# Optimization experiments

Hardware: AMD Instinct MI355X
Metric: run time of the kernel (lower is better)

The kernel has to match this reference:

```python
import jax, jax.numpy as jnp
import numpy as np

D_MODEL = 2048
N_HEADS = 16
N_KV_HEADS = 4
HEAD_DIM = D_MODEL // N_HEADS  # 128
SWA_WINDOW = 1024
SINK_TOKENS = 4
ROPE_BASE = 10000.0
EPS = 1e-6


def setup_inputs() -> dict:
    key = jax.random.key(0)
    ks = jax.random.split(key, 6)
    s = 0.02
    B, T = 1, 4096
    return {
        "x": jax.random.normal(ks[0], (B, T, D_MODEL), dtype=jnp.float32),
        "wq": jax.random.normal(ks[1], (N_HEADS * HEAD_DIM, D_MODEL), dtype=jnp.float32) * s,
        "wk": jax.random.normal(ks[2], (N_KV_HEADS * HEAD_DIM, D_MODEL), dtype=jnp.float32) * s,
        "wv": jax.random.normal(ks[3], (N_KV_HEADS * HEAD_DIM, D_MODEL), dtype=jnp.float32) * s,
        "wo": jax.random.normal(ks[4], (D_MODEL, D_MODEL), dtype=jnp.float32) * s,
        "qk_weight": jnp.ones((HEAD_DIM,), dtype=jnp.float32),
        "layer_idx": 1,
    }


def _rope_cos_sin(T, dtype):
    half = HEAD_DIM // 2
    inv_freq = 1.0 / (ROPE_BASE ** (jnp.arange(half, dtype=dtype) / half))
    freqs = jnp.arange(T, dtype=dtype)[:, None] * inv_freq[None, :]  # [T, half]
    return jnp.cos(freqs), jnp.sin(freqs)


def _rot(x, cos, sin):
    # x: [B,H,T,D]; cos/sin: [T,D/2]
    half = HEAD_DIM // 2
    x1, x2 = x[..., :half], x[..., half:]
    return jnp.concatenate([x1 * cos - x2 * sin, x1 * sin + x2 * cos], axis=-1)


def _qknorm(x, w):
    rms = jnp.sqrt(jnp.mean(x * x, axis=-1, keepdims=True) + EPS)
    return x / rms * w


def reference(x, wq, wk, wv, wo, qk_weight, layer_idx):
    B, T, C = x.shape
    rep = N_HEADS // N_KV_HEADS
    q = (x @ wq.T).reshape(B, T, N_HEADS, HEAD_DIM).transpose(0, 2, 1, 3)      # [B,H,T,D]
    k = (x @ wk.T).reshape(B, T, N_KV_HEADS, HEAD_DIM).transpose(0, 2, 1, 3)   # [B,Hkv,T,D]
    v = (x @ wv.T).reshape(B, T, N_KV_HEADS, HEAD_DIM).transpose(0, 2, 1, 3)
    k = jnp.repeat(k, rep, axis=1)  # GQA expand, matches repeat_interleave
    v = jnp.repeat(v, rep, axis=1)

    cos, sin = _rope_cos_sin(T, x.dtype)
    q = _rot(q, cos, sin)
    k = _rot(k, cos, sin)

    q = _qknorm(q, qk_weight)
    k = _qknorm(k, qk_weight)

    # sliding-window + sink mask (non-global layer). NOTE: faithful to the
    # original, which passes ~allowed as the boolean keep-mask to SDPA.
    i = jnp.arange(T)[:, None]
    j = jnp.arange(T)[None, :]
    allowed = (j <= i) & (((i - j) < SWA_WINDOW) | (j < SINK_TOKENS))
    keep = ~allowed  # True = attend (SDPA bool-mask semantics)

    scale = HEAD_DIM ** -0.5
    scores = jnp.einsum('bhqd,bhkd->bhqk', q, k) * scale
    scores = jnp.where(keep[None, None], scores, -jnp.inf)
    attn = jax.nn.softmax(scores, axis=-1)
    y = jnp.einsum('bhqk,bhkd->bhqd', attn, v)
    y = y.transpose(0, 2, 1, 3).reshape(B, T, C)
    return y @ wo.T
```

## Files before the change

kernel.cpp:

```cpp
#include <hip/hip_runtime.h>

typedef unsigned short u16;
typedef __bf16 bf16x8_t __attribute__((ext_vector_type(8)));
typedef float f32x4 __attribute__((ext_vector_type(4)));
typedef u16 u16x8 __attribute__((ext_vector_type(8)));
typedef u16 u16x4 __attribute__((ext_vector_type(4)));

__device__ __forceinline__ u16 f2bf(float f) {
  union { float f; unsigned u; } v; v.f = f;
  unsigned r = v.u + 0x7FFFu + ((v.u >> 16) & 1u);
  return (u16)(r >> 16);
}
__device__ __forceinline__ float bf2f(u16 b) {
  union { unsigned u; float f; } v; v.u = ((unsigned)b) << 16;
  return v.f;
}
__device__ __forceinline__ f32x4 mfma_bf16(u16x8 a, u16x8 b, f32x4 c) {
  return __builtin_amdgcn_mfma_f32_16x16x32_bf16(
      __builtin_bit_cast(bf16x8_t, a), __builtin_bit_cast(bf16x8_t, b), c, 0, 0, 0);
}

__global__ void k_cvt(const float* __restrict__ src, u16* __restrict__ dst, int n4) {
  int i = blockIdx.x * blockDim.x + threadIdx.x;
  if (i >= n4) return;
  float4 v = reinterpret_cast<const float4*>(src)[i];
  u16x4 o = { f2bf(v.x), f2bf(v.y), f2bf(v.z), f2bf(v.w) };
  reinterpret_cast<u16x4*>(dst)[i] = o;
}

template<bool BF16OUT>
__global__ __launch_bounds__(256, 2)
void k_gemm_bt(const u16* __restrict__ A, const u16* __restrict__ B,
               void* __restrict__ Cv, int M, int N, int K) {
  __shared__ u16 lA[128 * 64];
  __shared__ u16 lB[128 * 64];
  const int bm = blockIdx.y, bn = blockIdx.x;
  const int tid = threadIdx.x;
  const int wid = tid >> 6, lane = tid & 63;
  const int lo = lane & 15, hi = lane >> 4;
  const int wrow = (wid >> 1) * 64, wcol = (wid & 1) * 64;
  f32x4 acc[4][4] = {};
  const size_t abase = (size_t)(bm * 128) * K;
  const size_t bbase = (size_t)(bn * 128) * K;
  for (int kt = 0; kt < K; kt += 64) {
#pragma unroll
    for (int rr = 0; rr < 4; ++rr) {
      int e = (rr * 256 + tid) * 8;
      int row = e >> 6, col = e & 63;
      u16x8 va = *reinterpret_cast<const u16x8*>(A + abase + (size_t)row * K + kt + col);
      u16x8 vb = *reinterpret_cast<const u16x8*>(B + bbase + (size_t)row * K + kt + col);
      int sw = ((row * 64 + col) * 2) ^ ((row & 7) << 4);
      *reinterpret_cast<u16x8*>(reinterpret_cast<char*>(lA) + sw) = va;
      *reinterpret_cast<u16x8*>(reinterpret_cast<char*>(lB) + sw) = vb;
    }
    __syncthreads();
#pragma unroll
    for (int ks = 0; ks < 64; ks += 32) {
      u16x8 af[4], bfr[4];
#pragma unroll
      for (int mi = 0; mi < 4; ++mi) {
        int row = wrow + mi * 16 + lo, col = ks + hi * 8;
        int sw = ((row * 64 + col) * 2) ^ ((row & 7) << 4);
        af[mi] = *reinterpret_cast<const u16x8*>(reinterpret_cast<char*>(lA) + sw);
      }
#pragma unroll
      for (int ni = 0; ni < 4; ++ni) {
        int row = wcol + ni * 16 + lo, col = ks + hi * 8;
        int sw = ((row * 64 + col) * 2) ^ ((row & 7) << 4);
        bfr[ni] = *reinterpret_cast<const u16x8*>(reinterpret_cast<char*>(lB) + sw);
      }
#pragma unroll
      for (int mi = 0; mi < 4; ++mi)
#pragma unroll
        for (int ni = 0; ni < 4; ++ni)
          acc[mi][ni] = mfma_bf16(af[mi], bfr[ni], acc[mi][ni]);
    }
    __syncthreads();
  }
#pragma unroll
  for (int mi = 0; mi < 4; ++mi)
#pragma unroll
    for (int ni = 0; ni < 4; ++ni)
#pragma unroll
      for (int r = 0; r < 4; ++r) {
        int row = bm * 128 + wrow + mi * 16 + hi * 4 + r;
        int col = bn * 128 + wcol + ni * 16 + lo;
        if (BF16OUT)
          ((u16*)Cv)[(size_t)row * N + col] = f2bf(acc[mi][ni][r]);
        else
          ((float*)Cv)[(size_t)row * N + col] = acc[mi][ni][r];
      }
}

__global__ void k_rope_norm(const u16* __restrict__ QKV, const float* __restrict__ qkw,
                            u16* __restrict__ qb, u16* __restrict__ kb) {
  int gw = blockIdx.x * 4 + (threadIdx.x >> 6);
  int lane = threadIdx.x & 63;
  int t = gw / 20, hh = gw - t * 20;
  const u16* src = QKV + (size_t)t * 3072 + (hh < 16 ? hh * 128 : 2048 + (hh - 16) * 128);
  float x1 = bf2f(src[lane]), x2 = bf2f(src[lane + 64]);
  float invf = exp2f(-(float)lane * (13.287712379549449f / 64.0f));
  float fr = (float)t * invf;
  float sn, cs;
  sincosf(fr, &sn, &cs);
  float o1 = x1 * cs - x2 * sn, o2 = x1 * sn + x2 * cs;
  float ss = o1 * o1 + o2 * o2;
#pragma unroll
  for (int off = 32; off > 0; off >>= 1) ss += __shfl_xor(ss, off);
  float inv = rsqrtf(ss * (1.0f / 128.0f) + 1e-6f);
  o1 *= inv * qkw[lane];
  o2 *= inv * qkw[lane + 64];
  u16* dst = (hh < 16) ? (qb + ((size_t)hh * 4096 + t) * 128)
                       : (kb + ((size_t)(hh - 16) * 4096 + t) * 128);
  dst[lane] = f2bf(o1);
  dst[lane + 64] = f2bf(o2);
}

__global__ void k_transpose_v(const u16* __restrict__ QKV, u16* __restrict__ vtb) {
  __shared__ float lt[64][65];
  int b = blockIdx.x;
  int dt = b & 1, tt = (b >> 1) & 63, kv = b >> 7;
  int tid = threadIdx.x;
#pragma unroll
  for (int rr = 0; rr < 16; ++rr) {
    int row = rr * 4 + (tid >> 6);
    int col = tid & 63;
    lt[row][col] = bf2f(QKV[(size_t)(tt * 64 + row) * 3072 + 2560 + kv * 128 + dt * 64 + col]);
  }
  __syncthreads();
#pragma unroll
  for (int pp = 0; pp < 2; ++pp) {
    int idx = pp * 256 + tid;
    int dr = idx >> 3, tc = (idx & 7) * 8;
    u16x8 o;
#pragma unroll
    for (int i = 0; i < 8; ++i) o[i] = f2bf(lt[tc + i][dr]);
    *reinterpret_cast<u16x8*>(vtb + (size_t)(kv * 128 + dt * 64 + dr) * 4096 + tt * 64 + tc) = o;
  }
}

#define ATT_SL2E 0.12754276432973518f
#define ATT_SH   11.541560327111707f
#define KPAD 136
#define VPAD 40

__global__ __launch_bounds__(256)
void k_attn_mfma(const u16* __restrict__ qb, const u16* __restrict__ kb,
                 const u16* __restrict__ vtb, u16* __restrict__ yb) {
  __shared__ u16 sK[2][32][KPAD];
  __shared__ u16 sV[2][128][VPAD];
  const int h = blockIdx.y, qt = blockIdx.x;
  const int kvh = h >> 2;
  const int tid = threadIdx.x;
  const int wid = tid >> 6, lane = tid & 63;
  const int lo = lane & 15, hi = lane >> 4;
  const int q0 = qt * 128;
  const int qwA = q0 + wid * 16;
  const int qwB = qwA + 64;
  const int qrowA = qwA + lo, qrowB = qwB + lo;
  const u16* qpA = qb + ((size_t)h * 4096 + qrowA) * 128;
  const u16* qpB = qb + ((size_t)h * 4096 + qrowB) * 128;
  u16x8 qfA[4], qfB[4];
#pragma unroll
  for (int dc = 0; dc < 4; ++dc) {
    qfA[dc] = *reinterpret_cast<const u16x8*>(qpA + dc * 32 + hi * 8);
    qfB[dc] = *reinterpret_cast<const u16x8*>(qpB + dc * 32 + hi * 8);
  }
  f32x4 accOA[8] = {}, accOB[8] = {};
  float lsA = 0.0f, lsB = 0.0f;
  const u16* kbase = kb + (size_t)kvh * 4096 * 128;
  const u16* vb = vtb + (size_t)kvh * 128 * 4096;

  int past_tiles = 0;
  const int pe = q0 + 127 - 1024;
  if (pe >= 4) past_tiles = (pe >> 5) + 1;
  const int fstart = (q0 + 1) >> 5;
  const int ntiles = past_tiles + (128 - fstart);

  u16x8 kr[2], vr[2];
#define STAGE_LOAD(KT)                                                          \
  {                                                                             \
    const int kt_ = (KT);                                                       \
    _Pragma("unroll")                                                           \
    for (int p = 0; p < 2; ++p) {                                               \
      const int c = tid + p * 256;                                              \
      kr[p] = *reinterpret_cast<const u16x8*>(                                  \
          kbase + (size_t)(kt_ * 32 + (c >> 4)) * 128 + (c & 15) * 8);          \
      vr[p] = *reinterpret_cast<const u16x8*>(                                  \
          vb + (size_t)(c >> 2) * 4096 + kt_ * 32 + (c & 3) * 8);               \
    }                                                                           \
  }
#define STAGE_WRITE(BUF)                                                        \
  {                                                                             \
    const int b_ = (BUF);                                                       \
    _Pragma("unroll")                                                           \
    for (int p = 0; p < 2; ++p) {                                               \
      const int c = tid + p * 256;                                              \
      *reinterpret_cast<u16x8*>(&sK[b_][c >> 4][(c & 15) * 8]) = kr[p];         \
      const int d_ = c >> 2, a_ = c & 3;                                        \
      const int posA = ((a_ & 1) << 4) | ((a_ >> 1) << 2);                      \
      u16x4 v0_ = { vr[p][0], vr[p][1], vr[p][2], vr[p][3] };                   \
      u16x4 v1_ = { vr[p][4], vr[p][5], vr[p][6], vr[p][7] };                   \
      *reinterpret_cast<u16x4*>(&sV[b_][d_][posA]) = v0_;                       \
      *reinterpret_cast<u16x4*>(&sV[b_][d_][posA + 8]) = v1_;                   \
    }                                                                           \
  }

  STAGE_LOAD(0 < past_tiles ? 0 : fstart);
  STAGE_WRITE(0);
  __syncthreads();

  for (int i = 0; i < ntiles; ++i) {
    const int cur = i & 1;
    const int kt = (i < past_tiles) ? i : fstart + (i - past_tiles);
    const bool more = (i + 1) < ntiles;
    if (more) {
      const int i1 = i + 1;
      STAGE_LOAD((i1 < past_tiles) ? i1 : fstart + (i1 - past_tiles));
    }
    f32x4 aSA[2] = {}, aSB[2] = {};
#pragma unroll
    for (int sub = 0; sub < 2; ++sub)
#pragma unroll
      for (int dc = 0; dc < 4; ++dc) {
        u16x8 kf = *reinterpret_cast<const u16x8*>(&sK[cur][sub * 16 + lo][dc * 32 + hi * 8]);
        aSA[sub] = mfma_bf16(kf, qfA[dc], aSA[sub]);
        aSB[sub] = mfma_bf16(kf, qfB[dc], aSB[sub]);
      }
    u16x8 pfA, pfB;
#pragma unroll
    for (int sub = 0; sub < 2; ++sub)
#pragma unroll
      for (int r = 0; r < 4; ++r) {
        const int j = kt * 32 + sub * 16 + hi * 4 + r;
        float argA = aSA[sub][r] * ATT_SL2E - ATT_SH;
        float argB = aSB[sub][r] * ATT_SL2E - ATT_SH;
        const bool okA = (j > qrowA) || (((qrowA - j) >= 1024) && (j >= 4));
        const bool okB = (j > qrowB) || (((qrowB - j) >= 1024) && (j >= 4));
        argA = okA ? argA : -100000.0f;
        argB = okB ? argB : -100000.0f;
        float pA = exp2f(argA), pB = exp2f(argB);
        lsA += pA; lsB += pB;
        pfA[sub * 4 + r] = f2bf(pA);
        pfB[sub * 4 + r] = f2bf(pB);
      }
#pragma unroll
    for (int nt = 0; nt < 8; ++nt) {
      u16x8 vf = *reinterpret_cast<const u16x8*>(&sV[cur][nt * 16 + lo][hi * 8]);
      accOA[nt] = mfma_bf16(pfA, vf, accOA[nt]);
      accOB[nt] = mfma_bf16(pfB, vf, accOB[nt]);
    }
    if (more) STAGE_WRITE(cur ^ 1);
    __syncthreads();
  }
#undef STAGE_LOAD
#undef STAGE_WRITE

  lsA += __shfl_xor(lsA, 16); lsA += __shfl_xor(lsA, 32);
  lsB += __shfl_xor(lsB, 16); lsB += __shfl_xor(lsB, 32);
  float lrA[4], lrB[4];
#pragma unroll
  for (int r = 0; r < 4; ++r) {
    lrA[r] = 1.0f / __shfl(lsA, hi * 4 + r);
    lrB[r] = 1.0f / __shfl(lsB, hi * 4 + r);
  }
#pragma unroll
  for (int nt = 0; nt < 8; ++nt)
#pragma unroll
    for (int r = 0; r < 4; ++r) {
      const int tA = qwA + hi * 4 + r;
      const int tB = qwB + hi * 4 + r;
      yb[(size_t)tA * 2048 + h * 128 + nt * 16 + lo] = f2bf(accOA[nt][r] * lrA[r]);
      yb[(size_t)tB * 2048 + h * 128 + nt * 16 + lo] = f2bf(accOB[nt][r] * lrB[r]);
    }
}

extern "C" void kernel_launch(void* const* d_in, const int* in_sizes, int n_in,
                              void* d_out, int out_size, void* d_ws, size_t ws_size,
                              hipStream_t stream) {
  const float* x   = (const float*)d_in[0];
  const float* wq  = (const float*)d_in[1];
  const float* wk  = (const float*)d_in[2];
  const float* wv  = (const float*)d_in[3];
  const float* wo  = (const float*)d_in[4];
  const float* qkw = (const float*)d_in[5];
  (void)in_sizes; (void)n_in; (void)out_size; (void)ws_size;

  char* ws = (char*)d_ws;
  u16* xb    = (u16*)(ws);
  u16* wqkvb = (u16*)(ws + (16ull << 20));
  u16* wob   = (u16*)(ws + (28ull << 20));
  u16* qkvb  = (u16*)(ws + (36ull << 20));
  u16* qb    = (u16*)(ws + (60ull << 20));
  u16* kb    = (u16*)(ws + (76ull << 20));
  u16* vtb   = (u16*)(ws + (80ull << 20));
  u16* yb    = (u16*)(ws + (84ull << 20));

  k_cvt<<<8192, 256, 0, stream>>>(x, xb, 8388608 / 4);
  k_cvt<<<4096, 256, 0, stream>>>(wq, wqkvb, 4194304 / 4);
  k_cvt<<<1024, 256, 0, stream>>>(wk, wqkvb + 4194304, 1048576 / 4);
  k_cvt<<<1024, 256, 0, stream>>>(wv, wqkvb + 5242880, 1048576 / 4);
  k_cvt<<<4096, 256, 0, stream>>>(wo, wob, 4194304 / 4);

  k_gemm_bt<true><<<dim3(24, 32), 256, 0, stream>>>(xb, wqkvb, qkvb, 4096, 3072, 2048);
  k_rope_norm<<<20480, 256, 0, stream>>>(qkvb, qkw, qb, kb);
  k_transpose_v<<<512, 256, 0, stream>>>(qkvb, vtb);
  k_attn_mfma<<<dim3(32, 16), 256, 0, stream>>>(qb, kb, vtb, yb);
  k_gemm_bt<false><<<dim3(16, 32), 256, 0, stream>>>(yb, wob, (float*)d_out, 4096, 2048, 2048);
}
```

Measured before the change: 369.8 us.

## Split attention KV range across two blocks and merge partial sums

Adds a split-KV mode where each query tile's key range is divided between two blocks along grid z, each writing unnormalized fp32 partial outputs and row sums to workspace. A new merge kernel adds the two partials, normalizes, and writes bf16 output. This doubles attention grid parallelism and balances uneven tile counts, at the cost of extra fp32 global traffic and an additional launch. The split path is only taken when the workspace is large enough.

```diff
diff --git a/kernel.cpp b/kernel.cpp
--- a/kernel.cpp
+++ b/kernel.cpp
@@ -144,9 +144,11 @@
 #define KPAD 136
 #define VPAD 40
 
+template<bool SPLIT>
 __global__ __launch_bounds__(256)
 void k_attn_mfma(const u16* __restrict__ qb, const u16* __restrict__ kb,
-                 const u16* __restrict__ vtb, u16* __restrict__ yb) {
+                 const u16* __restrict__ vtb, u16* __restrict__ yb,
+                 float* __restrict__ P, float* __restrict__ L) {
   __shared__ u16 sK[2][32][KPAD];
   __shared__ u16 sV[2][128][VPAD];
   const int h = blockIdx.y, qt = blockIdx.x;
@@ -176,6 +178,12 @@
   if (pe >= 4) past_tiles = (pe >> 5) + 1;
   const int fstart = (q0 + 1) >> 5;
   const int ntiles = past_tiles + (128 - fstart);
+  int i0 = 0, i1 = ntiles;
+  if (SPLIT) {
+    const int half = blockIdx.z;
+    i0 = (half * ntiles) >> 1;
+    i1 = ((half + 1) * ntiles) >> 1;
+  }
 
   u16x8 kr[2], vr[2];
 #define STAGE_LOAD(KT)                                                          \
@@ -206,17 +214,17 @@
     }                                                                           \
   }
 
-  STAGE_LOAD(0 < past_tiles ? 0 : fstart);
+  STAGE_LOAD((i0 < past_tiles) ? i0 : fstart + (i0 - past_tiles));
   STAGE_WRITE(0);
   __syncthreads();
 
-  for (int i = 0; i < ntiles; ++i) {
-    const int cur = i & 1;
+  for (int i = i0; i < i1; ++i) {
+    const int cur = (i - i0) & 1;
     const int kt = (i < past_tiles) ? i : fstart + (i - past_tiles);
-    const bool more = (i + 1) < ntiles;
+    const bool more = (i + 1) < i1;
     if (more) {
-      const int i1 = i + 1;
-      STAGE_LOAD((i1 < past_tiles) ? i1 : fstart + (i1 - past_tiles));
+      const int i1n = i + 1;
+      STAGE_LOAD((i1n < past_tiles) ? i1n : fstart + (i1n - past_tiles));
     }
     f32x4 aSA[2] = {}, aSB[2] = {};
 #pragma unroll
@@ -258,21 +266,60 @@
 
   lsA += __shfl_xor(lsA, 16); lsA += __shfl_xor(lsA, 32);
   lsB += __shfl_xor(lsB, 16); lsB += __shfl_xor(lsB, 32);
-  float lrA[4], lrB[4];
-#pragma unroll
-  for (int r = 0; r < 4; ++r) {
-    lrA[r] = 1.0f / __shfl(lsA, hi * 4 + r);
-    lrB[r] = 1.0f / __shfl(lsB, hi * 4 + r);
-  }
-#pragma unroll
-  for (int nt = 0; nt < 8; ++nt)
+
+  if (!SPLIT) {
+    float lrA[4], lrB[4];
 #pragma unroll
     for (int r = 0; r < 4; ++r) {
-      const int tA = qwA + hi * 4 + r;
-      const int tB = qwB + hi * 4 + r;
-      yb[(size_t)tA * 2048 + h * 128 + nt * 16 + lo] = f2bf(accOA[nt][r] * lrA[r]);
-      yb[(size_t)tB * 2048 + h * 128 + nt * 16 + lo] = f2bf(accOB[nt][r] * lrB[r]);
-    }
+      lrA[r] = 1.0f / __shfl(lsA, hi * 4 + r);
+      lrB[r] = 1.0f / __shfl(lsB, hi * 4 + r);
+    }
+#pragma unroll
+    for (int nt = 0; nt < 8; ++nt)
+#pragma unroll
+      for (int r = 0; r < 4; ++r) {
+        const int tA = qwA + hi * 4 + r;
+        const int tB = qwB + hi * 4 + r;
+        yb[(size_t)tA * 2048 + h * 128 + nt * 16 + lo] = f2bf(accOA[nt][r] * lrA[r]);
+        yb[(size_t)tB * 2048 + h * 128 + nt * 16 + lo] = f2bf(accOB[nt][r] * lrB[r]);
+      }
+  } else {
+    const int half = blockIdx.z;
+    const size_t pbase = ((((size_t)half * 16 + h) * 32 + qt) * 16384);
+#pragma unroll
+    for (int nt = 0; nt < 8; ++nt)
+#pragma unroll
+      for (int r = 0; r < 4; ++r) {
+        const int qlA = wid * 16 + hi * 4 + r;
+        P[pbase + (size_t)qlA * 128 + nt * 16 + lo] = accOA[nt][r];
+        P[pbase + (size_t)(qlA + 64) * 128 + nt * 16 + lo] = accOB[nt][r];
+      }
+    if (hi == 0) {
+      const size_t lb = ((size_t)half * 16 + h) * 4096 + q0;
+      L[lb + wid * 16 + lo] = lsA;
+      L[lb + 64 + wid * 16 + lo] = lsB;
+    }
+  }
+}
+
+__global__ __launch_bounds__(256)
+void k_merge(const float* __restrict__ P, const float* __restrict__ L,
+             u16* __restrict__ yb) {
+  const int qt = blockIdx.x, h = blockIdx.y, tid = threadIdx.x;
+  const size_t b0 = (((size_t)0 * 16 + h) * 32 + qt) * 16384;
+  const size_t b1 = (((size_t)1 * 16 + h) * 32 + qt) * 16384;
+#pragma unroll
+  for (int it = 0; it < 16; ++it) {
+    const int g = it * 1024 + tid * 4;
+    const int ql = g >> 7, d = g & 127;
+    const int qg = qt * 128 + ql;
+    float4 p0 = *reinterpret_cast<const float4*>(P + b0 + g);
+    float4 p1 = *reinterpret_cast<const float4*>(P + b1 + g);
+    const float rl = 1.0f / (L[(size_t)h * 4096 + qg] + L[(size_t)65536 + h * 4096 + qg]);
+    u16x4 o = { f2bf((p0.x + p1.x) * rl), f2bf((p0.y + p1.y) * rl),
+                f2bf((p0.z + p1.z) * rl), f2bf((p0.w + p1.w) * rl) };
+    *reinterpret_cast<u16x4*>(yb + (size_t)qg * 2048 + h * 128 + d) = o;
+  }
 }
 
 extern "C" void kernel_launch(void* const* d_in, const int* in_sizes, int n_in,
@@ -284,7 +331,7 @@
   const float* wv  = (const float*)d_in[3];
   const float* wo  = (const float*)d_in[4];
   const float* qkw = (const float*)d_in[5];
-  (void)in_sizes; (void)n_in; (void)out_size; (void)ws_size;
+  (void)in_sizes; (void)n_in; (void)out_size;
 
   char* ws = (char*)d_ws;
   u16* xb    = (u16*)(ws);
@@ -295,6 +342,9 @@
   u16* kb    = (u16*)(ws + (76ull << 20));
   u16* vtb   = (u16*)(ws + (80ull << 20));
   u16* yb    = (u16*)(ws + (84ull << 20));
+  float* P   = (float*)(ws + (100ull << 20));
+  float* L   = (float*)(ws + (164ull << 20));
+  const bool split = ws_size >= (165ull << 20);
 
   k_cvt<<<8192, 256, 0, stream>>>(x, xb, 8388608 / 4);
   k_cvt<<<4096, 256, 0, stream>>>(wq, wqkvb, 4194304 / 4);
@@ -305,6 +355,11 @@
   k_gemm_bt<true><<<dim3(24, 32), 256, 0, stream>>>(xb, wqkvb, qkvb, 4096, 3072, 2048);
   k_rope_norm<<<20480, 256, 0, stream>>>(qkvb, qkw, qb, kb);
   k_transpose_v<<<512, 256, 0, stream>>>(qkvb, vtb);
-  k_attn_mfma<<<dim3(32, 16), 256, 0, stream>>>(qb, kb, vtb, yb);
+  if (split) {
+    k_attn_mfma<true><<<dim3(32, 16, 2), 256, 0, stream>>>(qb, kb, vtb, yb, P, L);
+    k_merge<<<dim3(32, 16), 256, 0, stream>>>(P, L, yb);
+  } else {
+    k_attn_mfma<false><<<dim3(32, 16, 1), 256, 0, stream>>>(qb, kb, vtb, yb, P, L);
+  }
   k_gemm_bt<false><<<dim3(16, 32), 256, 0, stream>>>(yb, wob, (float*)d_out, 4096, 2048, 2048);
 }
```

New measurement: 387.4 us. +4.8%, slower.
